# Optimization experiments

Measured on AMD Instinct MI355X. Metric: run time of the kernel, lower is better.

Reference implementation:

```python
import jax, jax.numpy as jnp
import numpy as np

N, C, E, H, K, GH, L = 50000, 256, 800000, 64, 32, 64, 2
EPS = 1e-8
LN_EPS = 1e-5


def setup_inputs() -> dict:
    key = jax.random.key(0)
    ks = jax.random.split(key, 24)
    s = lambda fan_in: 1.0 / np.sqrt(fan_in)
    inp = {
        "x": jax.random.normal(ks[0], (N, C), jnp.float32),
        "src": jax.random.randint(ks[1], (E,), 0, N),
        "dst": jax.random.randint(ks[2], (E,), 0, N),
        "base_w": jax.random.uniform(ks[3], (E,), jnp.float32),
        # encoder: Linear(C,H) -> ReLU -> Linear(H,H) -> ReLU  (weights stored [in,out])
        "enc_w1": jax.random.normal(ks[4], (C, H), jnp.float32) * s(C),
        "enc_b1": jnp.zeros((H,), jnp.float32),
        "enc_w2": jax.random.normal(ks[5], (H, H), jnp.float32) * s(H),
        "enc_b2": jnp.zeros((H,), jnp.float32),
        # edge gate: Linear(2H, GH) -> ReLU -> Linear(GH, 1) -> sigmoid
        "gate_w1": jax.random.normal(ks[6], (2 * H, GH), jnp.float32) * s(2 * H),
        "gate_b1": jnp.zeros((GH,), jnp.float32),
        "gate_w2": jax.random.normal(ks[7], (GH, 1), jnp.float32) * 0.1,
        "gate_b2": jnp.full((1,), 2.0, jnp.float32),
        # per-layer update MLPs (stacked over L layers): Linear(H,H)->ReLU->Linear(H,H)
        "upd_w1": jax.random.normal(ks[8], (L, H, H), jnp.float32) * s(H),
        "upd_b1": jnp.zeros((L, H), jnp.float32),
        "upd_w2": jax.random.normal(ks[9], (L, H, H), jnp.float32) * s(H),
        "upd_b2": jnp.zeros((L, H), jnp.float32),
        # per-layer LayerNorm params
        "ln_g": jnp.ones((L, H), jnp.float32),
        "ln_b": jnp.zeros((L, H), jnp.float32),
        # node reliability logits
        "rho_raw": jax.random.normal(ks[10], (N,), jnp.float32) * 0.1,
        # toU head: Linear(H, K)
        "toU_w": jax.random.normal(ks[11], (H, K), jnp.float32) * 0.1,
        "toU_b": jnp.ones((K,), jnp.float32),
    }
    return inp


def reference(x, src, dst, base_w,
              enc_w1, enc_b1, enc_w2, enc_b2,
              gate_w1, gate_b1, gate_w2, gate_b2,
              upd_w1, upd_b1, upd_w2, upd_b2,
              ln_g, ln_b, rho_raw, toU_w, toU_b):
    relu = jax.nn.relu
    # node encoder
    h = relu(relu(x @ enc_w1 + enc_b1) @ enc_w2 + enc_b2)  # [N, H]
    rho = jax.nn.sigmoid(rho_raw)                          # [N]
    rho_e = rho[src] * rho[dst]                            # [E]
    for l in range(L):
        h_src = h[src]                                     # [E, H] gather
        h_dst = h[dst]                                     # [E, H] gather
        z = relu(jnp.concatenate([h_src, h_dst], axis=1) @ gate_w1 + gate_b1)
        gate = jax.nn.sigmoid((z @ gate_w2 + gate_b2)[:, 0])  # [E]
        w = base_w * gate * rho_e                           # [E]
        # weighted scatter-add aggregate with degree normalization
        m = jax.ops.segment_sum(w[:, None] * h_src, dst, num_segments=N)  # [N, H]
        deg = jax.ops.segment_sum(w, dst, num_segments=N)                 # [N]
        neigh = m / (deg[:, None] + EPS)
        u = relu(neigh @ upd_w1[l] + upd_b1[l]) @ upd_w2[l] + upd_b2[l]
        pre = h + u
        mean = jnp.mean(pre, axis=-1, keepdims=True)
        var = jnp.var(pre, axis=-1, keepdims=True)
        h = (pre - mean) / jnp.sqrt(var + LN_EPS) * ln_g[l] + ln_b[l]
    U = jax.nn.softplus(h @ toU_w + toU_b)                 # [N, K]
    return U
```

## Files before the change

kernel.cpp:

```cpp
#include <hip/hip_runtime.h>
#include <math.h>


typedef unsigned short ushort_t;
typedef __attribute__((ext_vector_type(8))) short bf16x8;
typedef __attribute__((ext_vector_type(4))) float f32x4;

__device__ __forceinline__ float bf2f(ushort_t u) {
    return __uint_as_float(((unsigned int)u) << 16);
}
__device__ __forceinline__ ushort_t f2bf(float f) {
    unsigned int x = __float_as_uint(f);
    unsigned int lsb = (x >> 16) & 1u;
    x += 0x7fffu + lsb;
    return (ushort_t)(x >> 16);
}

__global__ __launch_bounds__(256) void pack_kernel(
    const float* __restrict__ w1, const float* __restrict__ w2,
    const float* __restrict__ gw1, const float* __restrict__ uw1,
    const float* __restrict__ uw2, const float* __restrict__ tw,
    ushort_t* __restrict__ w1f, ushort_t* __restrict__ w2f,
    ushort_t* __restrict__ g1f, ushort_t* __restrict__ u1f,
    ushort_t* __restrict__ u2f, ushort_t* __restrict__ tuf) {
    int t = blockIdx.x * 256 + threadIdx.x;
    if (t < 16384) {
        int i = t & 7, l = (t >> 3) & 63, kb = (t >> 9) & 7, nt = t >> 12;
        int k = kb * 32 + (l >> 4) * 8 + i, n = nt * 16 + (l & 15);
        w1f[t] = f2bf(w1[(size_t)k * 64 + n]);
    }
    if (t < 4096) {
        int i = t & 7, l = (t >> 3) & 63, kb = (t >> 9) & 1, nt = t >> 10;
        int k = kb * 32 + (l >> 4) * 8 + i, n = nt * 16 + (l & 15);
        w2f[t] = f2bf(w2[(size_t)k * 64 + n]);
    }
    if (t < 8192) {
        int i = t & 7, l = (t >> 3) & 63, kb = (t >> 9) & 1, j = t >> 10;
        int part = j >> 2, nt = j & 3;
        int k = part * 64 + kb * 32 + (l >> 4) * 8 + i, n = nt * 16 + (l & 15);
        g1f[t] = f2bf(gw1[(size_t)k * 64 + n]);
    }
    if (t < 8192) {
        int i = t & 7, l = (t >> 3) & 63, kb = (t >> 9) & 1;
        int nt = (t >> 10) & 3, lay = t >> 12;
        int k = kb * 32 + (l >> 4) * 8 + i, n = nt * 16 + (l & 15);
        u1f[t] = f2bf(uw1[(size_t)lay * 4096 + (size_t)k * 64 + n]);
        u2f[t] = f2bf(uw2[(size_t)lay * 4096 + (size_t)k * 64 + n]);
    }
    if (t < 2048) {
        int i = t & 7, l = (t >> 3) & 63, kb = (t >> 9) & 1, nt = t >> 10;
        int k = kb * 32 + (l >> 4) * 8 + i, n = nt * 16 + (l & 15);
        tuf[t] = f2bf(tw[(size_t)k * 32 + n]);
    }
}

__global__ __launch_bounds__(256) void enc_kernel(
    const float* __restrict__ x, const ushort_t* __restrict__ w1f,
    const float* __restrict__ b1, const ushort_t* __restrict__ w2f,
    const float* __restrict__ b2, const ushort_t* __restrict__ g1f,
    const float* __restrict__ gb1,
    ushort_t* __restrict__ ahb, float* __restrict__ bbuf, int N) {
    __shared__ ushort_t xls[16][264];
    __shared__ ushort_t tls[16][72];
    __shared__ ushort_t hls[16][72];
    __shared__ ushort_t als[16][72];
    __shared__ float    bls[16][68];
    const int tid  = threadIdx.x;
    const int lane = tid & 63;
    const int w    = tid >> 6;
    const int m    = lane & 15;
    const int g    = lane >> 4;
    const int rbase = blockIdx.x * 16;
    for (int p = tid; p < 16 * 64; p += 256) {
        int row = p >> 6, k4 = p & 63, grow = rbase + row;
        float4 v = (grow < N) ? *(const float4*)(x + (size_t)grow * 256 + k4 * 4)
                              : make_float4(0.f, 0.f, 0.f, 0.f);
        unsigned int p0 = (unsigned int)f2bf(v.x) | ((unsigned int)f2bf(v.y) << 16);
        unsigned int p1 = (unsigned int)f2bf(v.z) | ((unsigned int)f2bf(v.w) << 16);
        *(uint2*)&xls[row][k4 * 4] = make_uint2(p0, p1);
    }
    __syncthreads();
    f32x4 acc = {0, 0, 0, 0};
    #pragma unroll
    for (int kb = 0; kb < 8; ++kb) {
        bf16x8 a = *(const bf16x8*)&xls[m][kb * 32 + g * 8];
        bf16x8 b = *(const bf16x8*)(w1f + (((size_t)w * 8 + kb) * 64 + lane) * 8);
        acc = __builtin_amdgcn_mfma_f32_16x16x32_bf16(a, b, acc, 0, 0, 0);
    }
    {
        float bb1 = b1[w * 16 + m];
        #pragma unroll
        for (int r = 0; r < 4; ++r)
            tls[g * 4 + r][w * 16 + m] = f2bf(fmaxf(acc[r] + bb1, 0.f));
    }
    __syncthreads();
    f32x4 acc2 = {0, 0, 0, 0};
    #pragma unroll
    for (int kb = 0; kb < 2; ++kb) {
        bf16x8 a2 = *(const bf16x8*)&tls[m][kb * 32 + g * 8];
        bf16x8 b = *(const bf16x8*)(w2f + (((size_t)w * 2 + kb) * 64 + lane) * 8);
        acc2 = __builtin_amdgcn_mfma_f32_16x16x32_bf16(a2, b, acc2, 0, 0, 0);
    }
    {
        float bb2 = b2[w * 16 + m];
        #pragma unroll
        for (int r = 0; r < 4; ++r)
            hls[g * 4 + r][w * 16 + m] = f2bf(fmaxf(acc2[r] + bb2, 0.f));
    }
    __syncthreads();
    {
        int row = tid >> 4, c4 = tid & 15, grow = rbase + row;
        if (grow < N)
            *(ushort4*)(ahb + (size_t)grow * 128 + 64 + c4 * 4) =
                *(const ushort4*)&hls[row][c4 * 4];
    }
    f32x4 p0 = {0, 0, 0, 0}, p1 = {0, 0, 0, 0};
    #pragma unroll
    for (int kb = 0; kb < 2; ++kb) {
        bf16x8 a3 = *(const bf16x8*)&hls[m][kb * 32 + g * 8];
        bf16x8 b0 = *(const bf16x8*)(g1f + (((size_t)(2 * w) * 2 + kb) * 64 + lane) * 8);
        bf16x8 b1v = *(const bf16x8*)(g1f + (((size_t)(2 * w + 1) * 2 + kb) * 64 + lane) * 8);
        p0 = __builtin_amdgcn_mfma_f32_16x16x32_bf16(a3, b0, p0, 0, 0, 0);
        p1 = __builtin_amdgcn_mfma_f32_16x16x32_bf16(a3, b1v, p1, 0, 0, 0);
    }
    if (w < 2) {
        int j0 = 2 * w, j1 = 2 * w + 1;
        float gb0 = gb1[j0 * 16 + m], gb1v = gb1[j1 * 16 + m];
        #pragma unroll
        for (int r = 0; r < 4; ++r) {
            als[g * 4 + r][j0 * 16 + m] = f2bf(p0[r] + gb0);
            als[g * 4 + r][j1 * 16 + m] = f2bf(p1[r] + gb1v);
        }
    } else {
        int j0 = 2 * w - 4, j1 = 2 * w - 3;
        #pragma unroll
        for (int r = 0; r < 4; ++r) {
            bls[g * 4 + r][j0 * 16 + m] = p0[r];
            bls[g * 4 + r][j1 * 16 + m] = p1[r];
        }
    }
    __syncthreads();
    {
        int row = tid >> 4, c4 = tid & 15, grow = rbase + row;
        if (grow < N) {
            *(ushort4*)(ahb + (size_t)grow * 128 + c4 * 4) =
                *(const ushort4*)&als[row][c4 * 4];
            *(float4*)(bbuf + (size_t)grow * 64 + c4 * 4) =
                *(const float4*)&bls[row][c4 * 4];
        }
    }
}

__global__ __launch_bounds__(256) void hist_kernel(
    const int* __restrict__ dst, int* __restrict__ cnt,
    int* __restrict__ rank, int E) {
    for (int e = blockIdx.x * blockDim.x + threadIdx.x; e < E;
         e += gridDim.x * blockDim.x)
        rank[e] = atomicAdd(&cnt[dst[e]], 1);
}

__global__ __launch_bounds__(256) void scan1_kernel(
    const int* __restrict__ cnt, int* __restrict__ bsum, int N) {
    __shared__ int red[256];
    int i = blockIdx.x * 256 + threadIdx.x;
    red[threadIdx.x] = (i < N) ? cnt[i] : 0;
    __syncthreads();
    for (int off = 128; off > 0; off >>= 1) {
        if (threadIdx.x < off) red[threadIdx.x] += red[threadIdx.x + off];
        __syncthreads();
    }
    if (threadIdx.x == 0) bsum[blockIdx.x] = red[0];
}

__global__ __launch_bounds__(1024) void scan2_kernel(
    int* __restrict__ bsum, int nb) {
    __shared__ int s[1024];
    int v = (threadIdx.x < nb) ? bsum[threadIdx.x] : 0;
    s[threadIdx.x] = v;
    __syncthreads();
    for (int off = 1; off < 1024; off <<= 1) {
        int t = (threadIdx.x >= off) ? s[threadIdx.x - off] : 0;
        __syncthreads();
        s[threadIdx.x] += t;
        __syncthreads();
    }
    if (threadIdx.x < nb) bsum[threadIdx.x] = s[threadIdx.x] - v;
}

__global__ __launch_bounds__(256) void scan3_kernel(
    const int* __restrict__ cnt, const int* __restrict__ bsum,
    int* __restrict__ row_ptr, int N) {
    __shared__ int s[256];
    int i = blockIdx.x * 256 + threadIdx.x;
    int v = (i < N) ? cnt[i] : 0;
    s[threadIdx.x] = v;
    __syncthreads();
    for (int off = 1; off < 256; off <<= 1) {
        int t = (threadIdx.x >= off) ? s[threadIdx.x - off] : 0;
        __syncthreads();
        s[threadIdx.x] += t;
        __syncthreads();
    }
    if (i < N) row_ptr[i] = bsum[blockIdx.x] + s[threadIdx.x] - v;
    if (i == N - 1) row_ptr[N] = bsum[blockIdx.x] + s[threadIdx.x];
}

__global__ __launch_bounds__(256) void scatter_kernel(
    const int* __restrict__ src, const int* __restrict__ dst,
    const float* __restrict__ base_w, const float* __restrict__ rr,
    const int* __restrict__ row_ptr, const int* __restrict__ rank,
    int2* __restrict__ recs, int E) {
    for (int e = blockIdx.x * blockDim.x + threadIdx.x; e < E;
         e += gridDim.x * blockDim.x) {
        int s = src[e], d = dst[e];
        int pos = row_ptr[d] + rank[e];
        float rs = 1.f / (1.f + __expf(-rr[s]));
        float rd = 1.f / (1.f + __expf(-rr[d]));
        float c = base_w[e] * rs * rd;
        recs[pos] = make_int2(s, __float_as_int(c));
    }
}

__global__ __launch_bounds__(256) void gateagg_kernel(
    const int* __restrict__ row_ptr, const int2* __restrict__ recs,
    const ushort_t* __restrict__ ahb, const float* __restrict__ bb,
    const float* __restrict__ gw2, const float* __restrict__ gb2,
    ushort_t* __restrict__ nb, int N) {
    const int lane = threadIdx.x & 63;
    const int sub  = lane & 15;
    const int grp  = lane >> 4;
    const float4 gv = ((const float4*)gw2)[sub];
    const float gb = gb2[0];
    const int wid  = blockIdx.x * (blockDim.x >> 6) + (threadIdx.x >> 6);
    const int nw   = gridDim.x * (blockDim.x >> 6);
    for (int n = wid; n < N; n += nw) {
        const int beg = row_ptr[n], end = row_ptr[n + 1];
        const float4 bv = *(const float4*)(bb + (size_t)n * 64 + sub * 4);
        float m0 = 0.f, m1 = 0.f, m2 = 0.f, m3 = 0.f, dacc = 0.f;
        int i = beg + grp;
        for (; i + 4 < end; i += 8) {
            int2 rA = recs[i];
            int2 rB = recs[i + 4];
            const ushort_t* rowA = ahb + (size_t)rA.x * 128;
            const ushort_t* rowB = ahb + (size_t)rB.x * 128;
            ushort4 avA = *(const ushort4*)(rowA + sub * 4);
            ushort4 hvA = *(const ushort4*)(rowA + 64 + sub * 4);
            ushort4 avB = *(const ushort4*)(rowB + sub * 4);
            ushort4 hvB = *(const ushort4*)(rowB + 64 + sub * 4);
            float tA = fmaxf(bf2f(avA.x) + bv.x, 0.f) * gv.x
                     + fmaxf(bf2f(avA.y) + bv.y, 0.f) * gv.y
                     + fmaxf(bf2f(avA.z) + bv.z, 0.f) * gv.z
                     + fmaxf(bf2f(avA.w) + bv.w, 0.f) * gv.w;
            float tB = fmaxf(bf2f(avB.x) + bv.x, 0.f) * gv.x
                     + fmaxf(bf2f(avB.y) + bv.y, 0.f) * gv.y
                     + fmaxf(bf2f(avB.z) + bv.z, 0.f) * gv.z
                     + fmaxf(bf2f(avB.w) + bv.w, 0.f) * gv.w;
            #pragma unroll
            for (int o = 8; o > 0; o >>= 1) {
                tA += __shfl_xor(tA, o, 64);
                tB += __shfl_xor(tB, o, 64);
            }
            float wA = __int_as_float(rA.y) / (1.f + __expf(-(tA + gb)));
            float wB = __int_as_float(rB.y) / (1.f + __expf(-(tB + gb)));
            m0 = fmaf(wA, bf2f(hvA.x), m0); m0 = fmaf(wB, bf2f(hvB.x), m0);
            m1 = fmaf(wA, bf2f(hvA.y), m1); m1 = fmaf(wB, bf2f(hvB.y), m1);
            m2 = fmaf(wA, bf2f(hvA.z), m2); m2 = fmaf(wB, bf2f(hvB.z), m2);
            m3 = fmaf(wA, bf2f(hvA.w), m3); m3 = fmaf(wB, bf2f(hvB.w), m3);
            dacc += wA + wB;
        }
        if (i < end) {
            int2 r = recs[i];
            const ushort_t* row = ahb + (size_t)r.x * 128;
            ushort4 av = *(const ushort4*)(row + sub * 4);
            ushort4 hv = *(const ushort4*)(row + 64 + sub * 4);
            float t = fmaxf(bf2f(av.x) + bv.x, 0.f) * gv.x
                    + fmaxf(bf2f(av.y) + bv.y, 0.f) * gv.y
                    + fmaxf(bf2f(av.z) + bv.z, 0.f) * gv.z
                    + fmaxf(bf2f(av.w) + bv.w, 0.f) * gv.w;
            #pragma unroll
            for (int o = 8; o > 0; o >>= 1) t += __shfl_xor(t, o, 64);
            float w = __int_as_float(r.y) / (1.f + __expf(-(t + gb)));
            m0 = fmaf(w, bf2f(hv.x), m0);
            m1 = fmaf(w, bf2f(hv.y), m1);
            m2 = fmaf(w, bf2f(hv.z), m2);
            m3 = fmaf(w, bf2f(hv.w), m3);
            dacc += w;
        }
        #pragma unroll
        for (int o = 16; o < 64; o <<= 1) {
            m0 += __shfl_xor(m0, o, 64);
            m1 += __shfl_xor(m1, o, 64);
            m2 += __shfl_xor(m2, o, 64);
            m3 += __shfl_xor(m3, o, 64);
            dacc += __shfl_xor(dacc, o, 64);
        }
        if (lane < 16) {
            float dg = dacc + 1e-8f;
            ushort4 o4;
            o4.x = f2bf(m0 / dg);
            o4.y = f2bf(m1 / dg);
            o4.z = f2bf(m2 / dg);
            o4.w = f2bf(m3 / dg);
            *(ushort4*)(nb + (size_t)n * 64 + sub * 4) = o4;
        }
    }
}

template <int MODE>
__global__ __launch_bounds__(256) void upd_kernel(
    const ushort_t* __restrict__ nb,
    const ushort_t* __restrict__ u1f, const float* __restrict__ b1,
    const ushort_t* __restrict__ u2f, const float* __restrict__ b2,
    const float* __restrict__ lng, const float* __restrict__ lnb,
    const ushort_t* __restrict__ g1f, const float* __restrict__ gb1,
    ushort_t* __restrict__ ahb, float* __restrict__ bbuf,
    const ushort_t* __restrict__ tuf, const float* __restrict__ tub,
    float* __restrict__ U, int N) {
    __shared__ ushort_t xn[16][72];
    __shared__ ushort_t hls[16][72];
    __shared__ ushort_t tls[16][72];
    __shared__ ushort_t als[16][72];
    __shared__ float    bls[16][68];
    __shared__ float    sred[16][4][2];
    const int tid  = threadIdx.x;
    const int lane = tid & 63;
    const int w    = tid >> 6;
    const int m_   = lane & 15;
    const int g    = lane >> 4;
    const int rbase = blockIdx.x * 16;
    {
        int row = tid >> 4, c4 = tid & 15, grow = rbase + row;
        ushort4 z; z.x = z.y = z.z = z.w = 0;
        ushort4 nv = (grow < N) ? *(const ushort4*)(nb + (size_t)grow * 64 + c4 * 4) : z;
        ushort4 hv = (grow < N) ? *(const ushort4*)(ahb + (size_t)grow * 128 + 64 + c4 * 4) : z;
        *(ushort4*)&xn[row][c4 * 4] = nv;
        *(ushort4*)&hls[row][c4 * 4] = hv;
    }
    __syncthreads();
    f32x4 acc = {0, 0, 0, 0};
    #pragma unroll
    for (int kb = 0; kb < 2; ++kb) {
        bf16x8 a = *(const bf16x8*)&xn[m_][kb * 32 + g * 8];
        bf16x8 b = *(const bf16x8*)(u1f + (((size_t)w * 2 + kb) * 64 + lane) * 8);
        acc = __builtin_amdgcn_mfma_f32_16x16x32_bf16(a, b, acc, 0, 0, 0);
    }
    {
        float bb1 = b1[w * 16 + m_];
        #pragma unroll
        for (int r = 0; r < 4; ++r)
            tls[g * 4 + r][w * 16 + m_] = f2bf(fmaxf(acc[r] + bb1, 0.f));
    }
    __syncthreads();
    f32x4 acc2 = {0, 0, 0, 0};
    #pragma unroll
    for (int kb = 0; kb < 2; ++kb) {
        bf16x8 a2 = *(const bf16x8*)&tls[m_][kb * 32 + g * 8];
        bf16x8 b = *(const bf16x8*)(u2f + (((size_t)w * 2 + kb) * 64 + lane) * 8);
        acc2 = __builtin_amdgcn_mfma_f32_16x16x32_bf16(a2, b, acc2, 0, 0, 0);
    }
    float pre[4];
    {
        float bb2 = b2[w * 16 + m_];
        #pragma unroll
        for (int r = 0; r < 4; ++r) {
            pre[r] = acc2[r] + bb2 + bf2f(hls[g * 4 + r][w * 16 + m_]);
            float s1 = pre[r], s2 = pre[r] * pre[r];
            #pragma unroll
            for (int o = 1; o < 16; o <<= 1) {
                s1 += __shfl_xor(s1, o, 64);
                s2 += __shfl_xor(s2, o, 64);
            }
            if (m_ == 0) {
                sred[g * 4 + r][w][0] = s1;
                sred[g * 4 + r][w][1] = s2;
            }
        }
    }
    __syncthreads();
    {
        float lg = lng[w * 16 + m_], lb = lnb[w * 16 + m_];
        #pragma unroll
        for (int r = 0; r < 4; ++r) {
            int row = g * 4 + r;
            float s1 = (sred[row][0][0] + sred[row][1][0])
                     + (sred[row][2][0] + sred[row][3][0]);
            float s2 = (sred[row][0][1] + sred[row][1][1])
                     + (sred[row][2][1] + sred[row][3][1]);
            float mean = s1 * (1.0f / 64.0f);
            float var  = s2 * (1.0f / 64.0f) - mean * mean;
            float rinv = rsqrtf(var + 1e-5f);
            float hn = (pre[r] - mean) * rinv * lg + lb;
            tls[row][w * 16 + m_] = f2bf(hn);
        }
    }
    __syncthreads();
    if (MODE == 0) {
        {
            int row = tid >> 4, c4 = tid & 15, grow = rbase + row;
            if (grow < N)
                *(ushort4*)(ahb + (size_t)grow * 128 + 64 + c4 * 4) =
                    *(const ushort4*)&tls[row][c4 * 4];
        }
        f32x4 p0 = {0, 0, 0, 0}, p1 = {0, 0, 0, 0};
        #pragma unroll
        for (int kb = 0; kb < 2; ++kb) {
            bf16x8 a3 = *(const bf16x8*)&tls[m_][kb * 32 + g * 8];
            bf16x8 b0 = *(const bf16x8*)(g1f + (((size_t)(2 * w) * 2 + kb) * 64 + lane) * 8);
            bf16x8 b1v = *(const bf16x8*)(g1f + (((size_t)(2 * w + 1) * 2 + kb) * 64 + lane) * 8);
            p0 = __builtin_amdgcn_mfma_f32_16x16x32_bf16(a3, b0, p0, 0, 0, 0);
            p1 = __builtin_amdgcn_mfma_f32_16x16x32_bf16(a3, b1v, p1, 0, 0, 0);
        }
        if (w < 2) {
            int j0 = 2 * w, j1 = 2 * w + 1;
            float gb0 = gb1[j0 * 16 + m_], gb1v = gb1[j1 * 16 + m_];
            #pragma unroll
            for (int r = 0; r < 4; ++r) {
                als[g * 4 + r][j0 * 16 + m_] = f2bf(p0[r] + gb0);
                als[g * 4 + r][j1 * 16 + m_] = f2bf(p1[r] + gb1v);
            }
        } else {
            int j0 = 2 * w - 4, j1 = 2 * w - 3;
            #pragma unroll
            for (int r = 0; r < 4; ++r) {
                bls[g * 4 + r][j0 * 16 + m_] = p0[r];
                bls[g * 4 + r][j1 * 16 + m_] = p1[r];
            }
        }
        __syncthreads();
        {
            int row = tid >> 4, c4 = tid & 15, grow = rbase + row;
            if (grow < N) {
                *(ushort4*)(ahb + (size_t)grow * 128 + c4 * 4) =
                    *(const ushort4*)&als[row][c4 * 4];
                *(float4*)(bbuf + (size_t)grow * 64 + c4 * 4) =
                    *(const float4*)&bls[row][c4 * 4];
            }
        }
    } else {
        if (w < 2) {
            f32x4 au = {0, 0, 0, 0};
            #pragma unroll
            for (int kb = 0; kb < 2; ++kb) {
                bf16x8 a3 = *(const bf16x8*)&tls[m_][kb * 32 + g * 8];
                bf16x8 b = *(const bf16x8*)(tuf + (((size_t)w * 2 + kb) * 64 + lane) * 8);
                au = __builtin_amdgcn_mfma_f32_16x16x32_bf16(a3, b, au, 0, 0, 0);
            }
            float tb = tub[w * 16 + m_];
            #pragma unroll
            for (int r = 0; r < 4; ++r) {
                int grow = rbase + g * 4 + r;
                if (grow < N) {
                    float av = au[r] + tb;
                    float sp = av > 0.f ? av + log1pf(__expf(-av))
                                        : log1pf(__expf(av));
                    U[(size_t)grow * 32 + w * 16 + m_] = sp;
                }
            }
        }
    }
}

extern "C" void kernel_launch(void* const* d_in, const int* in_sizes, int n_in,
                              void* d_out, int out_size, void* d_ws, size_t ws_size,
                              hipStream_t stream) {
    const float* x       = (const float*)d_in[0];
    const int*   src     = (const int*)d_in[1];
    const int*   dst     = (const int*)d_in[2];
    const float* base_w  = (const float*)d_in[3];
    const float* enc_w1  = (const float*)d_in[4];
    const float* enc_b1  = (const float*)d_in[5];
    const float* enc_w2  = (const float*)d_in[6];
    const float* enc_b2  = (const float*)d_in[7];
    const float* gate_w1 = (const float*)d_in[8];
    const float* gate_b1 = (const float*)d_in[9];
    const float* gate_w2 = (const float*)d_in[10];
    const float* gate_b2 = (const float*)d_in[11];
    const float* upd_w1  = (const float*)d_in[12];
    const float* upd_b1  = (const float*)d_in[13];
    const float* upd_w2  = (const float*)d_in[14];
    const float* upd_b2  = (const float*)d_in[15];
    const float* ln_g    = (const float*)d_in[16];
    const float* ln_b    = (const float*)d_in[17];
    const float* rho_raw = (const float*)d_in[18];
    const float* toU_w   = (const float*)d_in[19];
    const float* toU_b   = (const float*)d_in[20];

    const int N = in_sizes[18];
    const int E = in_sizes[1];
    const int nsb = (N + 255) / 256;

    float* ws  = (float*)d_ws;
    size_t off = 0;
    ushort_t* ahb = (ushort_t*)(ws + off); off += (size_t)N * 64;
    float* bb  = ws + off; off += (size_t)N * 64;
    ushort_t* nb = (ushort_t*)(ws + off); off += (size_t)N * 32;
    int* row_ptr = (int*)(ws + off); off += (size_t)((N + 1 + 3) & ~3);
    int* cnt     = (int*)(ws + off); off += (size_t)((N + 3) & ~3);
    int* bsum    = (int*)(ws + off); off += (size_t)((nsb + 3) & ~3);
    int* rank    = (int*)(ws + off); off += (size_t)E;
    int2* recs   = (int2*)(ws + off); off += (size_t)E * 2;
    ushort_t* w1f = (ushort_t*)(ws + off); off += 8192;
    ushort_t* w2f = (ushort_t*)(ws + off); off += 2048;
    ushort_t* g1f = (ushort_t*)(ws + off); off += 4096;
    ushort_t* u1f = (ushort_t*)(ws + off); off += 4096;
    ushort_t* u2f = (ushort_t*)(ws + off); off += 4096;
    ushort_t* tuf = (ushort_t*)(ws + off); off += 1024;

    pack_kernel<<<64, 256, 0, stream>>>(enc_w1, enc_w2, gate_w1, upd_w1, upd_w2,
                                        toU_w, w1f, w2f, g1f, u1f, u2f, tuf);
    const int nblk16 = (N + 15) / 16;
    enc_kernel<<<nblk16, 256, 0, stream>>>(x, w1f, enc_b1, w2f, enc_b2,
                                           g1f, gate_b1, ahb, bb, N);

    hipMemsetAsync(cnt, 0, (size_t)N * sizeof(int), stream);
    hist_kernel<<<(E + 255) / 256, 256, 0, stream>>>(dst, cnt, rank, E);
    scan1_kernel<<<nsb, 256, 0, stream>>>(cnt, bsum, N);
    scan2_kernel<<<1, 1024, 0, stream>>>(bsum, nsb);
    scan3_kernel<<<nsb, 256, 0, stream>>>(cnt, bsum, row_ptr, N);
    scatter_kernel<<<(E + 255) / 256, 256, 0, stream>>>(src, dst, base_w, rho_raw,
                                                        row_ptr, rank, recs, E);

    gateagg_kernel<<<2048, 256, 0, stream>>>(row_ptr, recs, ahb, bb,
                                             gate_w2, gate_b2, nb, N);
    upd_kernel<0><<<nblk16, 256, 0, stream>>>(
        nb, u1f, upd_b1, u2f, upd_b2, ln_g, ln_b,
        g1f, gate_b1, ahb, bb, tuf, toU_b, (float*)d_out, N);

    gateagg_kernel<<<2048, 256, 0, stream>>>(row_ptr, recs, ahb, bb,
                                             gate_w2, gate_b2, nb, N);
    upd_kernel<1><<<nblk16, 256, 0, stream>>>(
        nb, u1f + 4096, upd_b1 + 64, u2f + 4096, upd_b2 + 64,
        ln_g + 64, ln_b + 64,
        g1f, gate_b1, ahb, bb, tuf, toU_b, (float*)d_out, N);
}
```

Measured before the change: 200.0 us.

## Interleave gate-activation and hidden features per node; precompute rho sigmoid once

Each node row in ahb now interleaves the 4 gate pre-activation values and 4 hidden values per 16-lane slot, so gateagg gathers both with one 16-byte load instead of two separate 8-byte loads from distant offsets. Producers in enc and upd kernels write the interleaved layout, and bf16 unpacking uses shift/mask directly. Separately, sigmoid(rho_raw) is computed once per node in a new small kernel rather than twice per edge in scatter. This adds one extra kernel launch.

```diff
diff --git a/kernel.cpp b/kernel.cpp
--- a/kernel.cpp
+++ b/kernel.cpp
@@ -52,6 +52,12 @@
         int k = kb * 32 + (l >> 4) * 8 + i, n = nt * 16 + (l & 15);
         tuf[t] = f2bf(tw[(size_t)k * 32 + n]);
     }
+}
+
+__global__ __launch_bounds__(256) void rho_kernel(
+    const float* __restrict__ rr, float* __restrict__ rho, int N) {
+    int i = blockIdx.x * 256 + threadIdx.x;
+    if (i < N) rho[i] = 1.f / (1.f + __expf(-rr[i]));
 }
 
 __global__ __launch_bounds__(256) void enc_kernel(
@@ -108,12 +114,6 @@
             hls[g * 4 + r][w * 16 + m] = f2bf(fmaxf(acc2[r] + bb2, 0.f));
     }
     __syncthreads();
-    {
-        int row = tid >> 4, c4 = tid & 15, grow = rbase + row;
-        if (grow < N)
-            *(ushort4*)(ahb + (size_t)grow * 128 + 64 + c4 * 4) =
-                *(const ushort4*)&hls[row][c4 * 4];
-    }
     f32x4 p0 = {0, 0, 0, 0}, p1 = {0, 0, 0, 0};
     #pragma unroll
     for (int kb = 0; kb < 2; ++kb) {
@@ -143,8 +143,10 @@
     {
         int row = tid >> 4, c4 = tid & 15, grow = rbase + row;
         if (grow < N) {
-            *(ushort4*)(ahb + (size_t)grow * 128 + c4 * 4) =
-                *(const ushort4*)&als[row][c4 * 4];
+            uint2 av = *(const uint2*)&als[row][c4 * 4];
+            uint2 hv = *(const uint2*)&hls[row][c4 * 4];
+            *(uint4*)(ahb + (size_t)grow * 128 + c4 * 8) =
+                make_uint4(av.x, av.y, hv.x, hv.y);
             *(float4*)(bbuf + (size_t)grow * 64 + c4 * 4) =
                 *(const float4*)&bls[row][c4 * 4];
         }
@@ -207,16 +209,14 @@
 
 __global__ __launch_bounds__(256) void scatter_kernel(
     const int* __restrict__ src, const int* __restrict__ dst,
-    const float* __restrict__ base_w, const float* __restrict__ rr,
+    const float* __restrict__ base_w, const float* __restrict__ rho,
     const int* __restrict__ row_ptr, const int* __restrict__ rank,
     int2* __restrict__ recs, int E) {
     for (int e = blockIdx.x * blockDim.x + threadIdx.x; e < E;
          e += gridDim.x * blockDim.x) {
         int s = src[e], d = dst[e];
         int pos = row_ptr[d] + rank[e];
-        float rs = 1.f / (1.f + __expf(-rr[s]));
-        float rd = 1.f / (1.f + __expf(-rr[d]));
-        float c = base_w[e] * rs * rd;
+        float c = base_w[e] * rho[s] * rho[d];
         recs[pos] = make_int2(s, __float_as_int(c));
     }
 }
@@ -241,20 +241,16 @@
         for (; i + 4 < end; i += 8) {
             int2 rA = recs[i];
             int2 rB = recs[i + 4];
-            const ushort_t* rowA = ahb + (size_t)rA.x * 128;
-            const ushort_t* rowB = ahb + (size_t)rB.x * 128;
-            ushort4 avA = *(const ushort4*)(rowA + sub * 4);
-            ushort4 hvA = *(const ushort4*)(rowA + 64 + sub * 4);
-            ushort4 avB = *(const ushort4*)(rowB + sub * 4);
-            ushort4 hvB = *(const ushort4*)(rowB + 64 + sub * 4);
-            float tA = fmaxf(bf2f(avA.x) + bv.x, 0.f) * gv.x
-                     + fmaxf(bf2f(avA.y) + bv.y, 0.f) * gv.y
-                     + fmaxf(bf2f(avA.z) + bv.z, 0.f) * gv.z
-                     + fmaxf(bf2f(avA.w) + bv.w, 0.f) * gv.w;
-            float tB = fmaxf(bf2f(avB.x) + bv.x, 0.f) * gv.x
-                     + fmaxf(bf2f(avB.y) + bv.y, 0.f) * gv.y
-                     + fmaxf(bf2f(avB.z) + bv.z, 0.f) * gv.z
-                     + fmaxf(bf2f(avB.w) + bv.w, 0.f) * gv.w;
+            uint4 pA = *(const uint4*)(ahb + (size_t)rA.x * 128 + sub * 8);
+            uint4 pB = *(const uint4*)(ahb + (size_t)rB.x * 128 + sub * 8);
+            float tA = fmaxf(__uint_as_float(pA.x << 16)         + bv.x, 0.f) * gv.x
+                     + fmaxf(__uint_as_float(pA.x & 0xffff0000u) + bv.y, 0.f) * gv.y
+                     + fmaxf(__uint_as_float(pA.y << 16)         + bv.z, 0.f) * gv.z
+                     + fmaxf(__uint_as_float(pA.y & 0xffff0000u) + bv.w, 0.f) * gv.w;
+            float tB = fmaxf(__uint_as_float(pB.x << 16)         + bv.x, 0.f) * gv.x
+                     + fmaxf(__uint_as_float(pB.x & 0xffff0000u) + bv.y, 0.f) * gv.y
+                     + fmaxf(__uint_as_float(pB.y << 16)         + bv.z, 0.f) * gv.z
+                     + fmaxf(__uint_as_float(pB.y & 0xffff0000u) + bv.w, 0.f) * gv.w;
             #pragma unroll
             for (int o = 8; o > 0; o >>= 1) {
                 tA += __shfl_xor(tA, o, 64);
@@ -262,28 +258,30 @@
             }
             float wA = __int_as_float(rA.y) / (1.f + __expf(-(tA + gb)));
             float wB = __int_as_float(rB.y) / (1.f + __expf(-(tB + gb)));
-            m0 = fmaf(wA, bf2f(hvA.x), m0); m0 = fmaf(wB, bf2f(hvB.x), m0);
-            m1 = fmaf(wA, bf2f(hvA.y), m1); m1 = fmaf(wB, bf2f(hvB.y), m1);
-            m2 = fmaf(wA, bf2f(hvA.z), m2); m2 = fmaf(wB, bf2f(hvB.z), m2);
-            m3 = fmaf(wA, bf2f(hvA.w), m3); m3 = fmaf(wB, bf2f(hvB.w), m3);
+            m0 = fmaf(wA, __uint_as_float(pA.z << 16), m0);
+            m1 = fmaf(wA, __uint_as_float(pA.z & 0xffff0000u), m1);
+            m2 = fmaf(wA, __uint_as_float(pA.w << 16), m2);
+            m3 = fmaf(wA, __uint_as_float(pA.w & 0xffff0000u), m3);
+            m0 = fmaf(wB, __uint_as_float(pB.z << 16), m0);
+            m1 = fmaf(wB, __uint_as_float(pB.z & 0xffff0000u), m1);
+            m2 = fmaf(wB, __uint_as_float(pB.w << 16), m2);
+            m3 = fmaf(wB, __uint_as_float(pB.w & 0xffff0000u), m3);
             dacc += wA + wB;
         }
         if (i < end) {
             int2 r = recs[i];
-            const ushort_t* row = ahb + (size_t)r.x * 128;
-            ushort4 av = *(const ushort4*)(row + sub * 4);
-            ushort4 hv = *(const ushort4*)(row + 64 + sub * 4);
-            float t = fmaxf(bf2f(av.x) + bv.x, 0.f) * gv.x
-                    + fmaxf(bf2f(av.y) + bv.y, 0.f) * gv.y
-                    + fmaxf(bf2f(av.z) + bv.z, 0.f) * gv.z
-                    + fmaxf(bf2f(av.w) + bv.w, 0.f) * gv.w;
+            uint4 p = *(const uint4*)(ahb + (size_t)r.x * 128 + sub * 8);
+            float t = fmaxf(__uint_as_float(p.x << 16)         + bv.x, 0.f) * gv.x
+                    + fmaxf(__uint_as_float(p.x & 0xffff0000u) + bv.y, 0.f) * gv.y
+                    + fmaxf(__uint_as_float(p.y << 16)         + bv.z, 0.f) * gv.z
+                    + fmaxf(__uint_as_float(p.y & 0xffff0000u) + bv.w, 0.f) * gv.w;
             #pragma unroll
             for (int o = 8; o > 0; o >>= 1) t += __shfl_xor(t, o, 64);
             float w = __int_as_float(r.y) / (1.f + __expf(-(t + gb)));
-            m0 = fmaf(w, bf2f(hv.x), m0);
-            m1 = fmaf(w, bf2f(hv.y), m1);
-            m2 = fmaf(w, bf2f(hv.z), m2);
-            m3 = fmaf(w, bf2f(hv.w), m3);
+            m0 = fmaf(w, __uint_as_float(p.z << 16), m0);
+            m1 = fmaf(w, __uint_as_float(p.z & 0xffff0000u), m1);
+            m2 = fmaf(w, __uint_as_float(p.w << 16), m2);
+            m3 = fmaf(w, __uint_as_float(p.w & 0xffff0000u), m3);
             dacc += w;
         }
         #pragma unroll
@@ -332,7 +330,7 @@
         int row = tid >> 4, c4 = tid & 15, grow = rbase + row;
         ushort4 z; z.x = z.y = z.z = z.w = 0;
         ushort4 nv = (grow < N) ? *(const ushort4*)(nb + (size_t)grow * 64 + c4 * 4) : z;
-        ushort4 hv = (grow < N) ? *(const ushort4*)(ahb + (size_t)grow * 128 + 64 + c4 * 4) : z;
+        ushort4 hv = (grow < N) ? *(const ushort4*)(ahb + (size_t)grow * 128 + c4 * 8 + 4) : z;
         *(ushort4*)&xn[row][c4 * 4] = nv;
         *(ushort4*)&hls[row][c4 * 4] = hv;
     }
@@ -395,12 +393,6 @@
     }
     __syncthreads();
     if (MODE == 0) {
-        {
-            int row = tid >> 4, c4 = tid & 15, grow = rbase + row;
-            if (grow < N)
-                *(ushort4*)(ahb + (size_t)grow * 128 + 64 + c4 * 4) =
-                    *(const ushort4*)&tls[row][c4 * 4];
-        }
         f32x4 p0 = {0, 0, 0, 0}, p1 = {0, 0, 0, 0};
         #pragma unroll
         for (int kb = 0; kb < 2; ++kb) {
@@ -430,8 +422,10 @@
         {
             int row = tid >> 4, c4 = tid & 15, grow = rbase + row;
             if (grow < N) {
-                *(ushort4*)(ahb + (size_t)grow * 128 + c4 * 4) =
-                    *(const ushort4*)&als[row][c4 * 4];
+                uint2 av = *(const uint2*)&als[row][c4 * 4];
+                uint2 hv = *(const uint2*)&tls[row][c4 * 4];
+                *(uint4*)(ahb + (size_t)grow * 128 + c4 * 8) =
+                    make_uint4(av.x, av.y, hv.x, hv.y);
                 *(float4*)(bbuf + (size_t)grow * 64 + c4 * 4) =
                     *(const float4*)&bls[row][c4 * 4];
             }
@@ -494,6 +488,7 @@
     ushort_t* ahb = (ushort_t*)(ws + off); off += (size_t)N * 64;
     float* bb  = ws + off; off += (size_t)N * 64;
     ushort_t* nb = (ushort_t*)(ws + off); off += (size_t)N * 32;
+    float* rho = ws + off; off += (size_t)((N + 3) & ~3);
     int* row_ptr = (int*)(ws + off); off += (size_t)((N + 1 + 3) & ~3);
     int* cnt     = (int*)(ws + off); off += (size_t)((N + 3) & ~3);
     int* bsum    = (int*)(ws + off); off += (size_t)((nsb + 3) & ~3);
@@ -508,6 +503,7 @@
 
     pack_kernel<<<64, 256, 0, stream>>>(enc_w1, enc_w2, gate_w1, upd_w1, upd_w2,
                                         toU_w, w1f, w2f, g1f, u1f, u2f, tuf);
+    rho_kernel<<<(N + 255) / 256, 256, 0, stream>>>(rho_raw, rho, N);
     const int nblk16 = (N + 15) / 16;
     enc_kernel<<<nblk16, 256, 0, stream>>>(x, w1f, enc_b1, w2f, enc_b2,
                                            g1f, gate_b1, ahb, bb, N);
@@ -517,7 +513,7 @@
     scan1_kernel<<<nsb, 256, 0, stream>>>(cnt, bsum, N);
     scan2_kernel<<<1, 1024, 0, stream>>>(bsum, nsb);
     scan3_kernel<<<nsb, 256, 0, stream>>>(cnt, bsum, row_ptr, N);
-    scatter_kernel<<<(E + 255) / 256, 256, 0, stream>>>(src, dst, base_w, rho_raw,
+    scatter_kernel<<<(E + 255) / 256, 256, 0, stream>>>(src, dst, base_w, rho,
                                                         row_ptr, rank, recs, E);
 
     gateagg_kernel<<<2048, 256, 0, stream>>>(row_ptr, recs, ahb, bb,
```

Result: no change. 201.5 us, median of 2 (+0.7%).
